# Performance work log

Measured on AMD Instinct MI355X. Metric: run time of the kernel, lower is better.

The kernel has to match this reference:

```python
import jax, jax.numpy as jnp
import numpy as np

B, S, N, D, NAMED, NTYPES = 8, 64, 100, 1024, 768, 5

def _ln(x, g, b, eps=1e-5):
    m = x.mean(-1, keepdims=True)
    v = ((x - m) ** 2).mean(-1, keepdims=True)
    return (x - m) * jax.lax.rsqrt(v + eps) * g + b

def _lin(x, W, b=None):
    y = x @ W.T
    return y if b is None else y + b

def setup_inputs():
    key = jax.random.key(0)
    ks = jax.random.split(key, 24)
    p = lambda i, shape, s=0.02: jax.random.normal(ks[i], shape, jnp.float32) * s
    inp = {}
    inp['scene_reps'] = jax.random.normal(ks[0], (B, S, D), jnp.float32)
    u = jax.random.uniform(ks[1], (B, N, S))
    keep = (jax.random.uniform(ks[2], (B, N, S)) < 0.25).astype(jnp.float32)
    inp['incidence_matrix'] = u * keep
    inp['edge_type_ids'] = jax.random.randint(ks[3], (B, S), 0, NTYPES)
    inp['entity_type_ids'] = jax.random.randint(ks[4], (B, N), 0, NTYPES)
    inp['entity_mask'] = jax.random.uniform(ks[5], (B, N)) < 0.9
    inp['entity_name_embs'] = jax.random.normal(ks[6], (B, N, NAMED), jnp.float32)
    inp['type_embed'] = p(7, (NTYPES, D), 1.0)
    inp['name_W'] = p(8, (D, NAMED))
    inp['name_ln_g'] = jnp.ones(D); inp['name_ln_b'] = jnp.zeros(D)
    inp['n2e_W'] = p(9, (D, D)); inp['n2e_b'] = jnp.zeros(D)
    inp['t2e_W'] = p(10, (D, D)); inp['t2e_b'] = jnp.zeros(D)
    inp['edge_ln_g'] = jnp.ones(D); inp['edge_ln_b'] = jnp.zeros(D)
    inp['gate_W1'] = p(11, (D // 4, D)); inp['gate_b1'] = jnp.zeros(D // 4)
    inp['gate_W2'] = p(12, (3, D // 4)); inp['gate_b2'] = jnp.zeros(3)
    inp['ms_W'] = p(13, (D, D)); inp['ms_b'] = jnp.zeros(D)
    inp['ma_W'] = p(14, (D, D)); inp['ma_b'] = jnp.zeros(D)
    inp['mi_W'] = p(15, (D, D)); inp['mi_b'] = jnp.zeros(D)
    inp['role_w'] = p(16, (D,))
    inp['gru_Wih'] = p(17, (3 * D, D)); inp['gru_Whh'] = p(18, (3 * D, D))
    inp['gru_bih'] = jnp.zeros(3 * D); inp['gru_bhh'] = jnp.zeros(3 * D)
    inp['upd_ln_g'] = jnp.ones(D); inp['upd_ln_b'] = jnp.zeros(D)
    inp['eo_W'] = p(19, (D, D)); inp['eo_b'] = jnp.zeros(D)
    inp['eo_ln_g'] = jnp.ones(D); inp['eo_ln_b'] = jnp.zeros(D)
    inp['res_ln_g'] = jnp.ones(D); inp['res_ln_b'] = jnp.zeros(D)
    return inp

def reference(scene_reps, incidence_matrix, edge_type_ids, entity_type_ids, entity_mask, entity_name_embs, type_embed, name_W, name_ln_g, name_ln_b, n2e_W, n2e_b, t2e_W, t2e_b, edge_ln_g, edge_ln_b, gate_W1, gate_b1, gate_W2, gate_b2, ms_W, ms_b, ma_W, ma_b, mi_W, mi_b, role_w, gru_Wih, gru_Whh, gru_bih, gru_bhh, upd_ln_g, upd_ln_b, eo_W, eo_b, eo_ln_g, eo_ln_b, res_ln_g, res_ln_b):
    # edge_type_ids is accepted by the torch module but unused in its forward.
    dt = scene_reps.dtype
    emaskf = entity_mask.astype(dt)  # [B,N]
    h0 = type_embed[entity_type_ids] + _ln(_lin(entity_name_embs, name_W), name_ln_g, name_ln_b)
    h0 = h0 * emaskf[..., None]
    eye = jnp.eye(N, dtype=dt)
    step_ids = jnp.arange(S)

    def step(carry, xs):
        h, ebuf = carry  # h [B,N,D], ebuf [B,S,D] (hyperedge history)
        s, x_s, inc_s = xs  # x_s [B,D], inc_s [B,N]
        roles = inc_s * emaskf
        wsum = jnp.maximum(roles.sum(1, keepdims=True), 1.0)
        mean_ent = jnp.einsum('bn,bnd->bd', roles, h) / wsum
        e_s = _ln(_lin(mean_ent, n2e_W, n2e_b) + _lin(x_s, t2e_W, t2e_b), edge_ln_g, edge_ln_b)
        in_mask = (roles > 0).astype(dt)[..., None]  # [B,N,1]
        msg_scene = _lin(e_s, ms_W, ms_b)[:, None, :]
        # arc stream: attention over past hyperedges with exponential recency decay
        valid = (step_ids < s).astype(dt)
        denom = jnp.maximum(s - 1, 1).astype(dt)
        decay = jnp.exp(-1.0 + step_ids.astype(dt) / denom) * valid  # linspace(-1,0,s)
        arc = incidence_matrix * roles[:, :, None] * decay[None, None, :]  # [B,N,S]
        arc = arc / jnp.maximum(arc.sum(-1, keepdims=True), 1e-8)
        msg_arc = _lin(jnp.einsum('bns,bsd->bnd', arc, jax.lax.stop_gradient(ebuf)), ma_W, ma_b)
        msg_arc = jnp.where(s > 0, msg_arc, jnp.zeros_like(msg_arc))
        # interaction stream: entity co-occurrence within the scene
        co = roles[:, :, None] * roles[:, None, :] * (1.0 - eye)
        co = co / jnp.maximum(co.sum(-1, keepdims=True), 1e-8)
        msg_int = _lin(jnp.einsum('bnm,bmd->bnd', co, h), mi_W, mi_b)
        gate = jax.nn.softmax(_lin(jax.nn.gelu(_lin(e_s, gate_W1, gate_b1), approximate=False), gate_W2, gate_b2), axis=-1)  # [B,3]
        msg = gate[:, 0, None, None] * msg_scene + gate[:, 1, None, None] * msg_arc + gate[:, 2, None, None] * msg_int
        msg = msg + (roles[..., None] * role_w) * in_mask
        # GRUCell (torch semantics) + LayerNorm, masked update
        gi = _lin(msg, gru_Wih, gru_bih)
        gh = _lin(h, gru_Whh, gru_bhh)
        i_r, i_z, i_n = jnp.split(gi, 3, axis=-1)
        h_r, h_z, h_n = jnp.split(gh, 3, axis=-1)
        r = jax.nn.sigmoid(i_r + h_r)
        z = jax.nn.sigmoid(i_z + h_z)
        n = jnp.tanh(i_n + r * h_n)
        h_new = jnp.clip(_ln((1 - z) * n + z * h, upd_ln_g, upd_ln_b), -50.0, 50.0)
        h = h * (1 - in_mask) + h_new * in_mask
        ebuf = ebuf.at[:, s].set(e_s)
        return (h, ebuf), e_s

    ebuf0 = jnp.zeros((B, S, D), dt)
    (h_fin, _), es = jax.lax.scan(step, (h0, ebuf0), (step_ids, scene_reps.transpose(1, 0, 2), incidence_matrix.transpose(2, 0, 1)))
    H = es.transpose(1, 0, 2)  # [B,S,D]
    H = _ln(H + scene_reps, res_ln_g, res_ln_b)
    H = _ln(jax.nn.gelu(_lin(H, eo_W, eo_b), approximate=False), eo_ln_g, eo_ln_b)
    return (H, h_fin)
```

## Files before the change

kernel.cpp:

```cpp
#include <hip/hip_runtime.h>
#include <math.h>

#define B_   8
#define S_   64
#define N_   100
#define D_   1024
#define ND_  768
#define BN_  800
#define G3_  3072
#define G6_  6144
#define RSC  0.00390625f

typedef _Float16 f16x8 __attribute__((ext_vector_type(8)));
typedef float f32x4 __attribute__((ext_vector_type(4)));

#define MFMA16(a,b,c) __builtin_amdgcn_mfma_f32_16x16x32_f16(a, b, c, 0, 0, 0)

static __device__ __forceinline__ float wave_sum(float v) {
    for (int off = 32; off > 0; off >>= 1) v += __shfl_down(v, off, 64);
    return v;
}

static __device__ __forceinline__ float block_sum(float v) {
    __shared__ float red_[8];
    float w = wave_sum(v);
    int lane = threadIdx.x & 63, wid = threadIdx.x >> 6;
    __syncthreads();
    if (lane == 0) red_[wid] = w;
    __syncthreads();
    float t = 0.f;
    for (int i = 0; i < 4; ++i) t += red_[i];
    return t;
}

static __device__ __forceinline__ float gelu_f(float x) {
    return 0.5f * x * (1.f + erff(x * 0.70710678118654752f));
}

static __device__ __forceinline__ unsigned short f2h(float x) {
    union { _Float16 h; unsigned short u; } c; c.h = (_Float16)x; return c.u;
}

__global__ __launch_bounds__(256) void k_f2h(
    const float* __restrict__ src, unsigned short* __restrict__ dst,
    int rows, int cols, int ldd)
{
    size_t n = (size_t)rows * cols;
    size_t i = ((size_t)blockIdx.x * 256 + threadIdx.x) * 4;
    if (i >= n) return;
    int r = (int)(i / cols);
    int c = (int)(i - (size_t)r * cols);
    float4 v = *(const float4*)(src + i);
    ushort4 o; o.x = f2h(v.x); o.y = f2h(v.y); o.z = f2h(v.z); o.w = f2h(v.w);
    *(ushort4*)(dst + (size_t)r * ldd + c) = o;
}

__global__ __launch_bounds__(256) void k_f2hT(
    const float* __restrict__ src, unsigned short* __restrict__ dst,
    int R, int C, int ldd, int rowoff)
{
    __shared__ _Float16 T[32][33];
    int tr = threadIdx.x >> 3, tc4 = (threadIdx.x & 7) * 4;
    int r0 = blockIdx.y * 32, c0 = blockIdx.x * 32;
    float4 v = *(const float4*)(src + (size_t)(r0 + tr) * C + c0 + tc4);
    T[tc4][tr] = (_Float16)v.x; T[tc4+1][tr] = (_Float16)v.y;
    T[tc4+2][tr] = (_Float16)v.z; T[tc4+3][tr] = (_Float16)v.w;
    __syncthreads();
    union { _Float16 h; unsigned short u; } cv;
    ushort4 o;
    cv.h = T[tr][tc4];   o.x = cv.u;
    cv.h = T[tr][tc4+1]; o.y = cv.u;
    cv.h = T[tr][tc4+2]; o.z = cv.u;
    cv.h = T[tr][tc4+3]; o.w = cv.u;
    *(ushort4*)(dst + (size_t)(rowoff + c0 + tr) * ldd + r0 + tc4) = o;
}

__global__ __launch_bounds__(256) void k_mfma16_nt(
    const unsigned short* __restrict__ A16, const unsigned short* __restrict__ W16,
    const float* __restrict__ bias, float* __restrict__ C,
    unsigned short* __restrict__ C16, float oscale,
    int M, int Nc, int K)
{
    int m0 = blockIdx.y * 64; if (m0 >= M) return;
    int n0 = blockIdx.x * 128;
    __shared__ _Float16 sA[64][72];
    __shared__ _Float16 sB[128][72];
    int tid = threadIdx.x;
    int w = tid >> 6, l = tid & 63;
    int l15 = l & 15, q = l >> 4;
    int wn = w * 32;
    int arow = tid >> 3, achk = (tid & 7) * 8;
    f32x4 acc[4][2] = {};
    for (int k0 = 0; k0 < K; k0 += 64) {
        for (int ri = 0; ri < 64; ri += 32) {
            int gm = m0 + arow + ri;
            uint4 v = make_uint4(0u, 0u, 0u, 0u);
            if (gm < M) v = *(const uint4*)(A16 + (size_t)gm * K + k0 + achk);
            *(uint4*)(&sA[arow + ri][achk]) = v;
        }
        for (int i = 0; i < 4; ++i) {
            int r = arow + 32 * i;
            *(uint4*)(&sB[r][achk]) = *(const uint4*)(W16 + (size_t)(n0 + r) * K + k0 + achk);
        }
        __syncthreads();
#pragma unroll
        for (int ks = 0; ks < 64; ks += 32) {
            f16x8 b0 = *(const f16x8*)(&sB[wn + l15][ks + q*8]);
            f16x8 b1 = *(const f16x8*)(&sB[wn + 16 + l15][ks + q*8]);
#pragma unroll
            for (int mi = 0; mi < 4; ++mi) {
                f16x8 a = *(const f16x8*)(&sA[mi*16 + l15][ks + q*8]);
                acc[mi][0] = MFMA16(a, b0, acc[mi][0]);
                acc[mi][1] = MFMA16(a, b1, acc[mi][1]);
            }
        }
        __syncthreads();
    }
    for (int mi = 0; mi < 4; ++mi)
        for (int nj = 0; nj < 2; ++nj)
            for (int r = 0; r < 4; ++r) {
                int gm = m0 + mi*16 + q*4 + r;
                int cl = wn + nj*16 + l15;
                if (gm < M) {
                    size_t off = (size_t)gm * Nc + n0 + cl;
                    float v = acc[mi][nj][r];
                    if (C16) C16[off] = f2h(v * oscale);
                    else C[off] = v + (bias ? bias[n0 + cl] : 0.f);
                }
            }
}

__global__ __launch_bounds__(256) void k_h0(
    const float* __restrict__ P, const int* __restrict__ etype,
    const int* __restrict__ emask, const float* __restrict__ temb,
    const float* __restrict__ g, const float* __restrict__ bt,
    float* __restrict__ h, unsigned short* __restrict__ h16)
{
    int bn = blockIdx.x, tid = threadIdx.x;
    int t = etype[bn], mk = emask[bn];
    float x[4]; float lsum = 0.f;
    for (int k = 0; k < 4; ++k) { x[k] = P[(size_t)bn*D_ + tid + 256*k]; lsum += x[k]; }
    float mean = block_sum(lsum) * (1.f / D_);
    float lv = 0.f;
    for (int k = 0; k < 4; ++k) { float d = x[k] - mean; lv += d * d; }
    float inv = rsqrtf(block_sum(lv) * (1.f / D_) + 1e-5f);
    for (int k = 0; k < 4; ++k) {
        int d = tid + 256*k;
        float y = (x[k] - mean) * inv * g[d] + bt[d];
        float hv = mk ? (temb[(size_t)t*D_ + d] + y) : 0.f;
        h[(size_t)bn*D_ + d] = hv;
        h16[(size_t)bn*D_ + d] = f2h(hv);
    }
}

__global__ __launch_bounds__(256) void k_step1(
    const float* __restrict__ inc, const int* __restrict__ emask,
    const float* __restrict__ h, const float* __restrict__ Esmi,
    float* __restrict__ ctxi, float* __restrict__ arcsum,
    int* __restrict__ cntp, int* __restrict__ lst, float* __restrict__ rro,
    const int* __restrict__ prevcnt, const int* __restrict__ prevlist,
    const unsigned short* __restrict__ h16, const unsigned short* __restrict__ n2e16,
    float* __restrict__ Hn, float* __restrict__ gatepre, int s)
{
    int tid = threadIdx.x, bid = blockIdx.x;
    if (bid == 0 && tid < 32) gatepre[tid] = 0.f;
    if (bid < BN_) {
        int m = bid;
        int b = m / N_, n = m - b * N_;
        float r = emask[m] ? inc[(size_t)m*S_ + s] : 0.f;
        if (r <= 0.f) return;
        __shared__ int sidx, nwa, nwi;
        __shared__ float wav[S_]; __shared__ int wai[S_];
        __shared__ float wiv[N_]; __shared__ int wii[N_];
        if (tid == 0) { sidx = atomicAdd(cntp, 1); nwa = 0; nwi = 0; }
        __syncthreads();
        int idx = sidx;
        if (tid == 0) { lst[idx] = m; rro[idx] = r; }
        float denomA = fmaxf((float)(s - 1), 1.f);
        float wa = 0.f;
        if (tid < s) {
            float iv = inc[(size_t)m*S_ + tid];
            if (iv > 0.f) {
                wa = iv * r * expf(-1.f + (float)tid / denomA);
                int p = atomicAdd(&nwa, 1);
                wav[p] = wa; wai[p] = tid;
            }
        }
        float dA = block_sum(wa);
        float wi = 0.f;
        if (tid < N_ && tid != n) {
            float rm = emask[b*N_ + tid] ? inc[((size_t)b*N_ + tid)*S_ + s] : 0.f;
            if (rm > 0.f) {
                wi = r * rm;
                int p = atomicAdd(&nwi, 1);
                wiv[p] = wi; wii[p] = tid;
            }
        }
        float dI = block_sum(wi);
        __syncthreads();
        int na = nwa, ni = nwi;
        float sclA = 1.f / fmaxf(dA, 1e-8f);
        float sclI = 1.f / fmaxf(dI, 1e-8f);
        float4 ii = make_float4(0.f,0.f,0.f,0.f);
        for (int j = 0; j < ni; ++j) {
            float wj = wiv[j];
            float4 v = *((const float4*)(h + ((size_t)b*N_ + wii[j])*D_) + tid);
            ii.x += wj*v.x; ii.y += wj*v.y; ii.z += wj*v.z; ii.w += wj*v.w;
        }
        ii.x *= sclI; ii.y *= sclI; ii.z *= sclI; ii.w *= sclI;
        *((float4*)(ctxi + (size_t)idx*D_) + tid) = ii;
        float a12[12];
#pragma unroll
        for (int k = 0; k < 12; ++k) a12[k] = 0.f;
        for (int j = 0; j < na; ++j) {
            float wj = wav[j];
            const float* ep = Esmi + ((size_t)b*S_ + wai[j])*G3_;
#pragma unroll
            for (int k = 0; k < 12; ++k) a12[k] += wj * ep[tid + 256*k];
        }
        float* ao = arcsum + (size_t)idx*G3_;
#pragma unroll
        for (int k = 0; k < 12; ++k) ao[tid + 256*k] = a12[k] * sclA;
    } else {
        int pM = *prevcnt;
        int t = bid - BN_;
        int n0 = (t & 15) * 64;
        int m0 = (t >> 4) * 32;
        if (m0 >= pM) return;
        __shared__ _Float16 sA[32][72];
        __shared__ _Float16 sB[64][72];
        __shared__ int slist[32];
        if (tid < 32) {
            int gm = m0 + tid;
            slist[tid] = (gm < pM) ? prevlist[gm] : 0;
        }
        __syncthreads();
        int w = tid >> 6, l = tid & 63;
        int l15 = l & 15, q = l >> 4;
        int wm = (w & 1) * 16, wn = (w >> 1) * 32;
        int arow = tid >> 3, achk = (tid & 7) * 8;
        int gmA = m0 + arow;
        f32x4 acc[2] = {};
        for (int k0 = 0; k0 < D_; k0 += 64) {
            {
                uint4 v = make_uint4(0u,0u,0u,0u);
                if (gmA < pM) v = *(const uint4*)(h16 + (size_t)slist[arow]*D_ + k0 + achk);
                *(uint4*)(&sA[arow][achk]) = v;
            }
            *(uint4*)(&sB[arow][achk])      = *(const uint4*)(n2e16 + (size_t)(n0 + arow)*D_ + k0 + achk);
            *(uint4*)(&sB[arow + 32][achk]) = *(const uint4*)(n2e16 + (size_t)(n0 + arow + 32)*D_ + k0 + achk);
            __syncthreads();
#pragma unroll
            for (int ks = 0; ks < 64; ks += 32) {
                f16x8 a  = *(const f16x8*)(&sA[wm + l15][ks + q*8]);
                f16x8 b0 = *(const f16x8*)(&sB[wn + l15][ks + q*8]);
                f16x8 b1 = *(const f16x8*)(&sB[wn + 16 + l15][ks + q*8]);
                acc[0] = MFMA16(a, b0, acc[0]);
                acc[1] = MFMA16(a, b1, acc[1]);
            }
            __syncthreads();
        }
        for (int j = 0; j < 2; ++j)
            for (int r = 0; r < 4; ++r) {
                int row = wm + q*4 + r;
                int gm = m0 + row;
                if (gm < pM)
                    Hn[(size_t)slist[row]*D_ + n0 + wn + j*16 + l15] = acc[j][r];
            }
    }
}

__global__ __launch_bounds__(256) void k_egate(
    const float* __restrict__ inc, const int* __restrict__ emask,
    const float* __restrict__ Hn, const float* __restrict__ n2eb,
    const float* __restrict__ pre_t2e,
    const float* __restrict__ elng, const float* __restrict__ elnb,
    const float* __restrict__ gW1, const float* __restrict__ gb1,
    const float* __restrict__ gW2,
    float* __restrict__ esbuf, float* __restrict__ gatepre,
    int* __restrict__ ctrl, int par, int s)
{
    int b = blockIdx.x, seg = blockIdx.y, tid = threadIdx.x;
    if (b == 0 && seg == 0 && tid == 0) ctrl[1 - par] = 0;
    __shared__ float sw[N_]; __shared__ int sidxn[N_]; __shared__ int snact;
    __shared__ float se[D_];
    if (tid == 0) snact = 0;
    __syncthreads();
    float r = 0.f;
    if (tid < N_) {
        r = emask[b*N_ + tid] ? inc[((size_t)b*N_ + tid)*S_ + s] : 0.f;
        if (r > 0.f) {
            int p = atomicAdd(&snact, 1);
            sw[p] = r; sidxn[p] = tid;
        }
    }
    float wsum = block_sum(r);
    int nact = snact;
    float invw = 1.f / fmaxf(wsum, 1.f);
    float4 e = make_float4(0.f,0.f,0.f,0.f);
    for (int j = 0; j < nact; ++j) {
        float wj = sw[j];
        float4 v = *((const float4*)(Hn + ((size_t)b*N_ + sidxn[j])*D_) + tid);
        e.x += wj*v.x; e.y += wj*v.y; e.z += wj*v.z; e.w += wj*v.w;
    }
    float4 nb = *((const float4*)n2eb + tid);
    float4 pt = *((const float4*)(pre_t2e + ((size_t)b*S_ + s)*D_) + tid);
    float x[4];
    x[0] = e.x*invw + nb.x + pt.x; x[1] = e.y*invw + nb.y + pt.y;
    x[2] = e.z*invw + nb.z + pt.z; x[3] = e.w*invw + nb.w + pt.w;
    float lsum = x[0] + x[1] + x[2] + x[3];
    float mean = block_sum(lsum) * (1.f / D_);
    float lv = 0.f;
    for (int k = 0; k < 4; ++k) { float d = x[k] - mean; lv += d * d; }
    float inv = rsqrtf(block_sum(lv) * (1.f / D_) + 1e-5f);
    float4 lg = *((const float4*)elng + tid);
    float4 lb = *((const float4*)elnb + tid);
    float y0 = (x[0]-mean)*inv*lg.x + lb.x;
    float y1 = (x[1]-mean)*inv*lg.y + lb.y;
    float y2 = (x[2]-mean)*inv*lg.z + lb.z;
    float y3 = (x[3]-mean)*inv*lg.w + lb.w;
    int d4 = tid * 4;
    se[d4] = y0; se[d4+1] = y1; se[d4+2] = y2; se[d4+3] = y3;
    if (seg == 0)
        *((float4*)(esbuf + ((size_t)b*S_ + s)*D_) + tid) = make_float4(y0,y1,y2,y3);
    __syncthreads();
    if (tid < 64) {
        int u = seg * 64 + tid;
        float acc = gb1[u];
        const float* w1 = gW1 + (size_t)u * D_;
        for (int j = 0; j < D_; j += 4) {
            float4 w = *(const float4*)(w1 + j);
            acc += w.x*se[j] + w.y*se[j+1] + w.z*se[j+2] + w.w*se[j+3];
        }
        float hg = gelu_f(acc);
        for (int c = 0; c < 3; ++c) {
            float p = wave_sum(gW2[c*256 + u] * hg);
            if (tid == 0) atomicAdd(gatepre + b*4 + c, p);
        }
    }
}

__global__ __launch_bounds__(256) void k_gemm_step(
    const float* __restrict__ ctxi, const float* __restrict__ esbuf,
    const unsigned short* __restrict__ h16,
    const int* __restrict__ lst, const int* __restrict__ cntp,
    const float* __restrict__ gatepre, const float* __restrict__ gb2,
    const unsigned short* __restrict__ Wmi16, const unsigned short* __restrict__ Whh16,
    const float* __restrict__ bhh, float* __restrict__ gig,
    float* __restrict__ Emi, float* __restrict__ Esmi, int s)
{
    int M = *cntp;
    int X = blockIdx.x, tid = threadIdx.x;
    int kind = (X < 48) ? 0 : (X < 96 ? 1 : 2);
    int m0 = blockIdx.y * 32;
    if (kind < 2) { if (m0 >= M) return; }
    else { if (blockIdx.y != 0) return; m0 = 0; }
    __shared__ _Float16 sA[32][72];
    __shared__ _Float16 sB[64][72];
    __shared__ float sg2[32];
    __shared__ int sbb[32];
    if (tid < 32) {
        int gm = m0 + tid;
        if (kind == 0) {
            float g2 = 0.f; int b = 0;
            if (gm < M) {
                b = lst[gm] / N_;
                float t0 = gatepre[b*4+0] + gb2[0];
                float t1 = gatepre[b*4+1] + gb2[1];
                float t2 = gatepre[b*4+2] + gb2[2];
                float mx = fmaxf(t0, fmaxf(t1, t2));
                float e0 = expf(t0-mx), e1 = expf(t1-mx), e2 = expf(t2-mx);
                g2 = e2 / (e0 + e1 + e2);
            }
            sg2[tid] = g2; sbb[tid] = b;
        } else if (kind == 1) {
            sbb[tid] = (gm < M) ? lst[gm] : 0;
        }
    }
    __syncthreads();
    int w = tid >> 6, l = tid & 63;
    int l15 = l & 15, q = l >> 4;
    int wm = (w & 1) * 16, wn = (w >> 1) * 32;
    int arow = tid >> 3, achk = (tid & 7) * 8;
    int gmA = m0 + arow;
    const unsigned short* Bp;
    int n0, ldb;
    if (kind == 0)      { n0 = X * 64;          Bp = Wmi16 + 2048; ldb = G3_; }
    else if (kind == 1) { n0 = (X - 48) * 64;   Bp = Whh16;        ldb = D_;  }
    else { int xo = X - 96; n0 = (xo % 48) * 64; Bp = Wmi16 + (xo / 48) * 1024; ldb = G3_; }
    f32x4 acc[2] = {};
    for (int k0 = 0; k0 < D_; k0 += 64) {
        {
            uint4 va = make_uint4(0u,0u,0u,0u);
            if (kind == 0) {
                if (gmA < M) {
                    float4 p0 = *(const float4*)(ctxi + (size_t)gmA*D_ + k0 + achk);
                    float4 p1 = *(const float4*)(ctxi + (size_t)gmA*D_ + k0 + achk + 4);
                    float sc = sg2[arow];
                    union { _Float16 hh[8]; uint4 u; } cv;
                    cv.hh[0] = (_Float16)(p0.x*sc); cv.hh[1] = (_Float16)(p0.y*sc);
                    cv.hh[2] = (_Float16)(p0.z*sc); cv.hh[3] = (_Float16)(p0.w*sc);
                    cv.hh[4] = (_Float16)(p1.x*sc); cv.hh[5] = (_Float16)(p1.y*sc);
                    cv.hh[6] = (_Float16)(p1.z*sc); cv.hh[7] = (_Float16)(p1.w*sc);
                    va = cv.u;
                }
            } else if (kind == 1) {
                if (gmA < M) va = *(const uint4*)(h16 + (size_t)sbb[arow]*D_ + k0 + achk);
            } else {
                if (arow < B_) {
                    const float* base = esbuf + ((size_t)arow*S_ + s)*D_ + k0 + achk;
                    float4 p0 = *(const float4*)(base);
                    float4 p1 = *(const float4*)(base + 4);
                    union { _Float16 hh[8]; uint4 u; } cv;
                    cv.hh[0] = (_Float16)p0.x; cv.hh[1] = (_Float16)p0.y;
                    cv.hh[2] = (_Float16)p0.z; cv.hh[3] = (_Float16)p0.w;
                    cv.hh[4] = (_Float16)p1.x; cv.hh[5] = (_Float16)p1.y;
                    cv.hh[6] = (_Float16)p1.z; cv.hh[7] = (_Float16)p1.w;
                    va = cv.u;
                }
            }
            *(uint4*)(&sA[arow][achk]) = va;
        }
        *(uint4*)(&sB[arow][achk])      = *(const uint4*)(Bp + (size_t)(n0 + arow)*ldb + k0 + achk);
        *(uint4*)(&sB[arow + 32][achk]) = *(const uint4*)(Bp + (size_t)(n0 + arow + 32)*ldb + k0 + achk);
        __syncthreads();
#pragma unroll
        for (int ks = 0; ks < 64; ks += 32) {
            f16x8 a  = *(const f16x8*)(&sA[wm + l15][ks + q*8]);
            f16x8 b0 = *(const f16x8*)(&sB[wn + l15][ks + q*8]);
            f16x8 b1 = *(const f16x8*)(&sB[wn + 16 + l15][ks + q*8]);
            acc[0] = MFMA16(a, b0, acc[0]);
            acc[1] = MFMA16(a, b1, acc[1]);
        }
        __syncthreads();
    }
    for (int j = 0; j < 2; ++j)
        for (int r = 0; r < 4; ++r) {
            int row = wm + q*4 + r;
            int gm = m0 + row;
            int cl = wn + j*16 + l15;
            if (kind == 0) {
                if (gm < M) gig[(size_t)gm * G6_ + n0 + cl] = acc[j][r];
            } else if (kind == 1) {
                if (gm < M) gig[(size_t)gm * G6_ + G3_ + n0 + cl] = acc[j][r] + bhh[n0 + cl];
            } else {
                if (row < B_) {
                    int xo = X - 96;
                    if (xo < 48) Emi[(size_t)row * G3_ + n0 + cl] = acc[j][r];
                    else Esmi[((size_t)row * S_ + s) * G3_ + n0 + cl] = acc[j][r];
                }
            }
        }
}

__global__ __launch_bounds__(256) void k_fin(
    const float* __restrict__ gig,
    const int* __restrict__ lst, const int* __restrict__ cntp,
    const float* __restrict__ ulng, const float* __restrict__ ulnb,
    const float* __restrict__ Emi, const float* __restrict__ arcsum,
    const float* __restrict__ gatepre, const float* __restrict__ gb2,
    const float* __restrict__ gBm, const float* __restrict__ bih,
    const float* __restrict__ rro,
    float* __restrict__ h, unsigned short* __restrict__ h16, int s)
{
    int row = blockIdx.x;
    if (row >= *cntp) return;
    int bn = lst[row];
    int b = bn / N_;
    int tid = threadIdx.x;
    float t0 = gatepre[b*4+0] + gb2[0];
    float t1 = gatepre[b*4+1] + gb2[1];
    float t2 = gatepre[b*4+2] + gb2[2];
    float mx = fmaxf(t0, fmaxf(t1, t2));
    float e0 = expf(t0-mx), e1 = expf(t1-mx), e2 = expf(t2-mx);
    float si = 1.f / (e0 + e1 + e2);
    float g0 = e0*si, g1 = (s > 0) ? e1*si : 0.f, g2 = e2*si;
    float rv = rro[row];
    const float* gi = gig + (size_t)row * G6_;
    const float* gh = gi + G3_;
    const float* em = Emi + (size_t)b * G3_;
    const float* as = arcsum + (size_t)row * G3_;
    float u[4]; float lsum = 0.f;
    for (int k = 0; k < 4; ++k) {
        int d = tid + 256*k;
        float ip[3];
#pragma unroll
        for (int c = 0; c < 3; ++c) {
            int dd = c*D_ + d;
            ip[c] = RSC * (gi[dd] + g0*em[dd] + g1*as[dd])
                  + g0*gBm[dd] + g1*gBm[G3_ + dd] + g2*gBm[2*G3_ + dd]
                  + rv*gBm[3*G3_ + dd] + bih[dd];
        }
        float hr = gh[d], hz = gh[D_ + d], hn = gh[2*D_ + d];
        float hv = h[(size_t)bn*D_ + d];
        float r = 1.f / (1.f + expf(-(ip[0] + hr)));
        float z = 1.f / (1.f + expf(-(ip[1] + hz)));
        float nn = tanhf(ip[2] + r * hn);
        u[k] = (1.f - z) * nn + z * hv;
        lsum += u[k];
    }
    float mean = block_sum(lsum) * (1.f / D_);
    float lv = 0.f;
    for (int k = 0; k < 4; ++k) { float d = u[k] - mean; lv += d * d; }
    float inv = rsqrtf(block_sum(lv) * (1.f / D_) + 1e-5f);
    for (int k = 0; k < 4; ++k) {
        int d = tid + 256*k;
        float y = (u[k] - mean) * inv * ulng[d] + ulnb[d];
        y = fminf(fmaxf(y, -50.f), 50.f);
        h[(size_t)bn*D_ + d] = y;
        h16[(size_t)bn*D_ + d] = f2h(y);
    }
}

__global__ __launch_bounds__(256) void k_resln(
    float* __restrict__ buf, const float* __restrict__ scene,
    const float* __restrict__ g, const float* __restrict__ bt,
    unsigned short* __restrict__ H16)
{
    size_t row = blockIdx.x;
    int tid = threadIdx.x;
    float x[4]; float lsum = 0.f;
    for (int k = 0; k < 4; ++k) {
        int d = tid + 256*k;
        x[k] = buf[row*D_ + d] + scene[row*D_ + d];
        lsum += x[k];
    }
    float mean = block_sum(lsum) * (1.f / D_);
    float lv = 0.f;
    for (int k = 0; k < 4; ++k) { float d = x[k] - mean; lv += d * d; }
    float inv = rsqrtf(block_sum(lv) * (1.f / D_) + 1e-5f);
    for (int k = 0; k < 4; ++k) {
        int d = tid + 256*k;
        float y = (x[k] - mean) * inv * g[d] + bt[d];
        buf[row*D_ + d] = y;
        H16[row*D_ + d] = f2h(y);
    }
}

__global__ __launch_bounds__(256) void k_final(
    const float* __restrict__ G, const float* __restrict__ g, const float* __restrict__ bt,
    float* __restrict__ outH, const float* __restrict__ h, float* __restrict__ outh)
{
    int tid = threadIdx.x;
    if (blockIdx.x < B_*S_) {
        size_t row = blockIdx.x;
        float x[4]; float lsum = 0.f;
        for (int k = 0; k < 4; ++k) {
            x[k] = gelu_f(G[row*D_ + tid + 256*k]);
            lsum += x[k];
        }
        float mean = block_sum(lsum) * (1.f / D_);
        float lv = 0.f;
        for (int k = 0; k < 4; ++k) { float d = x[k] - mean; lv += d * d; }
        float inv = rsqrtf(block_sum(lv) * (1.f / D_) + 1e-5f);
        for (int k = 0; k < 4; ++k) {
            int d = tid + 256*k;
            outH[row*D_ + d] = (x[k] - mean) * inv * g[d] + bt[d];
        }
    } else {
        size_t bn = blockIdx.x - B_*S_;
        for (int d = tid; d < D_; d += 256)
            outh[bn*D_ + d] = h[bn*D_ + d];
    }
}

extern "C" void kernel_launch(void* const* d_in, const int* in_sizes, int n_in,
                              void* d_out, int out_size, void* d_ws, size_t ws_size,
                              hipStream_t stream)
{
    const float* scene = (const float*)d_in[0];
    const float* inc   = (const float*)d_in[1];
    const int*   etype = (const int*)d_in[3];
    const int*   emask = (const int*)d_in[4];
    const float* nemb  = (const float*)d_in[5];
    const float* temb  = (const float*)d_in[6];
    const float* nameW = (const float*)d_in[7];
    const float* nlg   = (const float*)d_in[8];
    const float* nlb   = (const float*)d_in[9];
    const float* n2eW  = (const float*)d_in[10];
    const float* n2eb  = (const float*)d_in[11];
    const float* t2eW  = (const float*)d_in[12];
    const float* t2eb  = (const float*)d_in[13];
    const float* elng  = (const float*)d_in[14];
    const float* elnb  = (const float*)d_in[15];
    const float* gW1   = (const float*)d_in[16];
    const float* gb1   = (const float*)d_in[17];
    const float* gW2   = (const float*)d_in[18];
    const float* gb2   = (const float*)d_in[19];
    const float* msW   = (const float*)d_in[20];
    const float* msB   = (const float*)d_in[21];
    const float* maW   = (const float*)d_in[22];
    const float* maB   = (const float*)d_in[23];
    const float* miW   = (const float*)d_in[24];
    const float* miB   = (const float*)d_in[25];
    const float* rolew = (const float*)d_in[26];
    const float* Wih   = (const float*)d_in[27];
    const float* Whh   = (const float*)d_in[28];
    const float* bih   = (const float*)d_in[29];
    const float* bhh   = (const float*)d_in[30];
    const float* ulng  = (const float*)d_in[31];
    const float* ulnb  = (const float*)d_in[32];
    const float* eoW   = (const float*)d_in[33];
    const float* eoB   = (const float*)d_in[34];
    const float* eolng = (const float*)d_in[35];
    const float* eolnb = (const float*)d_in[36];
    const float* rlng  = (const float*)d_in[37];
    const float* rlnb  = (const float*)d_in[38];

    float* outH = (float*)d_out;
    float* outh = outH + (size_t)B_*S_*D_;

    float* W = (float*)d_ws;
    size_t o = 0;
    int*   ctrl     = (int*)(W + o); o += 64;
    float* gatepre  = W + o; o += 32;
    float* rowrole  = W + o; o += 2*BN_;
    int*   list     = (int*)(W + o); o += 2*BN_;
    float* ctxi     = W + o; o += (size_t)BN_*D_;
    float* hbuf     = W + o; o += (size_t)BN_*D_;
    float* Hn       = W + o; o += (size_t)BN_*D_;
    float* pre_t2e  = W + o; o += (size_t)B_*S_*D_;
    float* gBm      = W + o; o += 4*G3_;
    float* Emi      = W + o; o += (size_t)B_*G3_;
    float* Esmi     = W + o; o += (size_t)B_*S_*G3_;
    float* arcsum   = W + o; o += (size_t)BN_*G3_;
    float* gig      = W + o; o += (size_t)BN_*G6_;
    unsigned short* U = (unsigned short*)(W + o);
    size_t uo = 0;
    unsigned short* h16    = U + uo; uo += (size_t)BN_*D_;
    unsigned short* H16    = U + uo; uo += (size_t)B_*S_*D_;
    unsigned short* Wih16  = U + uo; uo += (size_t)G3_*D_;
    unsigned short* Whh16  = U + uo; uo += (size_t)G3_*D_;
    unsigned short* n2e16  = U + uo; uo += (size_t)D_*D_;
    unsigned short* eoW16  = U + uo; uo += (size_t)D_*D_;
    unsigned short* nW16   = U + uo; uo += (size_t)D_*ND_;
    unsigned short* nE16   = U + uo; uo += (size_t)BN_*ND_;
    unsigned short* t2e16  = U + uo; uo += (size_t)D_*D_;
    unsigned short* sc16   = U + uo; uo += (size_t)B_*S_*D_;
    unsigned short* WcatT16= U + uo; uo += (size_t)G3_*D_;
    unsigned short* Wmi16  = U + uo; uo += (size_t)G3_*G3_;
    unsigned short* bias4  = U + uo; uo += 4*D_;

    hipMemsetAsync(ctrl, 0, 16, stream);

    #define CVT(src, dst, r, c, ld) \
        k_f2h<<<(((size_t)(r)*(c)/4 + 255)/256), 256, 0, stream>>>(src, dst, r, c, ld)
    CVT(Wih,   Wih16, G3_, D_,  D_);
    CVT(Whh,   Whh16, G3_, D_,  D_);
    CVT(n2eW,  n2e16, D_,  D_,  D_);
    CVT(nameW, nW16,  D_,  ND_, ND_);
    CVT(nemb,  nE16,  BN_, ND_, ND_);
    CVT(eoW,   eoW16, D_,  D_,  D_);
    CVT(t2eW,  t2e16, D_,  D_,  D_);
    CVT(scene, sc16,  B_*S_, D_, D_);
    CVT(msB,   bias4 + 0,    1, D_, D_);
    CVT(maB,   bias4 + D_,   1, D_, D_);
    CVT(miB,   bias4 + 2*D_, 1, D_, D_);
    CVT(rolew, bias4 + 3*D_, 1, D_, D_);
    #undef CVT
    k_f2hT<<<dim3(32,32), 256, 0, stream>>>(msW, WcatT16, D_, D_, D_, 0);
    k_f2hT<<<dim3(32,32), 256, 0, stream>>>(maW, WcatT16, D_, D_, D_, D_);
    k_f2hT<<<dim3(32,32), 256, 0, stream>>>(miW, WcatT16, D_, D_, D_, 2*D_);

    k_mfma16_nt<<<dim3(G3_/128, G3_/64), 256, 0, stream>>>(
        Wih16, WcatT16, nullptr, nullptr, Wmi16, 256.f, G3_, G3_, D_);
    k_mfma16_nt<<<dim3(G3_/128, 1), 256, 0, stream>>>(
        bias4, Wih16, nullptr, gBm, nullptr, 1.f, 4, G3_, D_);
    k_mfma16_nt<<<dim3(D_/128, (B_*S_+63)/64), 256, 0, stream>>>(
        sc16, t2e16, t2eb, pre_t2e, nullptr, 1.f, B_*S_, D_, D_);
    k_mfma16_nt<<<dim3(D_/128, (BN_+63)/64), 256, 0, stream>>>(
        nE16, nW16, nullptr, gig, nullptr, 1.f, BN_, D_, ND_);
    k_h0<<<BN_, 256, 0, stream>>>(gig, etype, emask, temb, nlg, nlb, hbuf, h16);
    k_mfma16_nt<<<dim3(D_/128, (BN_+63)/64), 256, 0, stream>>>(
        h16, n2e16, nullptr, Hn, nullptr, 1.f, BN_, D_, D_);

    for (int s = 0; s < S_; ++s) {
        int par = s & 1;
        int*   cntp = ctrl + par;
        int*   pcnt = ctrl + (1 - par);
        int*   lst  = list + par * BN_;
        int*   plst = list + (1 - par) * BN_;
        float* rro  = rowrole + par * BN_;
        k_step1<<<BN_ + 400, 256, 0, stream>>>(inc, emask, hbuf, Esmi,
            ctxi, arcsum, cntp, lst, rro, pcnt, plst, h16, n2e16, Hn, gatepre, s);
        k_egate<<<dim3(B_, 4), 256, 0, stream>>>(inc, emask, Hn, n2eb, pre_t2e,
            elng, elnb, gW1, gb1, gW2, outH, gatepre, ctrl, par, s);
        k_gemm_step<<<dim3(192, 25), 256, 0, stream>>>(ctxi, outH, h16,
            lst, cntp, gatepre, gb2, Wmi16, Whh16, bhh, gig, Emi, Esmi, s);
        k_fin<<<BN_, 256, 0, stream>>>(gig, lst, cntp, ulng, ulnb,
            Emi, arcsum, gatepre, gb2, gBm, bih, rro, hbuf, h16, s);
    }

    k_resln<<<B_*S_, 256, 0, stream>>>(outH, scene, rlng, rlnb, H16);
    k_mfma16_nt<<<dim3(D_/128, (B_*S_+63)/64), 256, 0, stream>>>(
        H16, eoW16, eoB, gig, nullptr, 1.f, B_*S_, D_, D_);
    k_final<<<B_*S_ + BN_, 256, 0, stream>>>(gig, eolng, eolnb, outH, hbuf, outh);
}
```

Baseline: 5.018 ms.

## Precompute per-entity h projections and replace interaction context with batch sum minus self

The per-entity projection of h now covers n2e, the interaction slice of the merged msg-to-GRU weight, and Whh in one concatenated 7168-wide output (Hcat). It is refreshed only for the rows updated in the previous step, inside the front kernel. The interaction message term becomes a per-batch weighted sum of projected rows minus the entity's own contribution, with scaling done in k_fin. This removes the per-step ctxi gather and the separate gemm_step kernel, cutting four launches per step to three. In exchange the incremental GEMM is wider (112 column tiles), and precision shifts because the interaction term is projected before weighting rather than after.

```diff
diff --git a/kernel.cpp b/kernel.cpp
--- a/kernel.cpp
+++ b/kernel.cpp
@@ -9,6 +9,7 @@
 #define BN_  800
 #define G3_  3072
 #define G6_  6144
+#define HC7  7168
 #define RSC  0.00390625f
 
 typedef _Float16 f16x8 __attribute__((ext_vector_type(8)));
@@ -153,29 +154,70 @@
     }
 }
 
-__global__ __launch_bounds__(256) void k_step1(
+__global__ __launch_bounds__(256) void k_hcat0(
+    const unsigned short* __restrict__ h16, const unsigned short* __restrict__ n2e16,
+    const unsigned short* __restrict__ Wmi16, const unsigned short* __restrict__ Whh16,
+    float* __restrict__ Hcat)
+{
+    int m0 = blockIdx.y * 32;
+    int n0 = blockIdx.x * 64;
+    const unsigned short* Bp; int ldb; int nl;
+    if (n0 < 1024)      { Bp = n2e16;        ldb = D_;  nl = n0; }
+    else if (n0 < 4096) { Bp = Wmi16 + 2048; ldb = G3_; nl = n0 - 1024; }
+    else                { Bp = Whh16;        ldb = D_;  nl = n0 - 4096; }
+    __shared__ _Float16 sA[32][72];
+    __shared__ _Float16 sB[64][72];
+    int tid = threadIdx.x;
+    int w = tid >> 6, l = tid & 63;
+    int l15 = l & 15, q = l >> 4;
+    int wm = (w & 1) * 16, wn = (w >> 1) * 32;
+    int arow = tid >> 3, achk = (tid & 7) * 8;
+    int gmA = m0 + arow;
+    f32x4 acc[2] = {};
+    for (int k0 = 0; k0 < D_; k0 += 64) {
+        *(uint4*)(&sA[arow][achk]) = *(const uint4*)(h16 + (size_t)gmA*D_ + k0 + achk);
+        *(uint4*)(&sB[arow][achk])      = *(const uint4*)(Bp + (size_t)(nl + arow)*ldb + k0 + achk);
+        *(uint4*)(&sB[arow + 32][achk]) = *(const uint4*)(Bp + (size_t)(nl + arow + 32)*ldb + k0 + achk);
+        __syncthreads();
+#pragma unroll
+        for (int ks = 0; ks < 64; ks += 32) {
+            f16x8 a  = *(const f16x8*)(&sA[wm + l15][ks + q*8]);
+            f16x8 b0 = *(const f16x8*)(&sB[wn + l15][ks + q*8]);
+            f16x8 b1 = *(const f16x8*)(&sB[wn + 16 + l15][ks + q*8]);
+            acc[0] = MFMA16(a, b0, acc[0]);
+            acc[1] = MFMA16(a, b1, acc[1]);
+        }
+        __syncthreads();
+    }
+    for (int j = 0; j < 2; ++j)
+        for (int r = 0; r < 4; ++r) {
+            int row = wm + q*4 + r;
+            Hcat[(size_t)(m0 + row)*HC7 + n0 + wn + j*16 + l15] = acc[j][r];
+        }
+}
+
+__global__ __launch_bounds__(256) void k_front(
     const float* __restrict__ inc, const int* __restrict__ emask,
-    const float* __restrict__ h, const float* __restrict__ Esmi,
-    float* __restrict__ ctxi, float* __restrict__ arcsum,
+    const float* __restrict__ Esmi, float* __restrict__ arcsum,
     int* __restrict__ cntp, int* __restrict__ lst, float* __restrict__ rro,
+    float* __restrict__ scl,
     const int* __restrict__ prevcnt, const int* __restrict__ prevlist,
     const unsigned short* __restrict__ h16, const unsigned short* __restrict__ n2e16,
-    float* __restrict__ Hn, float* __restrict__ gatepre, int s)
+    const unsigned short* __restrict__ Wmi16, const unsigned short* __restrict__ Whh16,
+    float* __restrict__ Hcat, float* __restrict__ gatepre, int s)
 {
     int tid = threadIdx.x, bid = blockIdx.x;
     if (bid == 0 && tid < 32) gatepre[tid] = 0.f;
     if (bid < BN_) {
         int m = bid;
-        int b = m / N_, n = m - b * N_;
+        int b = m / N_;
         float r = emask[m] ? inc[(size_t)m*S_ + s] : 0.f;
         if (r <= 0.f) return;
-        __shared__ int sidx, nwa, nwi;
+        __shared__ int sidx, nwa;
         __shared__ float wav[S_]; __shared__ int wai[S_];
-        __shared__ float wiv[N_]; __shared__ int wii[N_];
-        if (tid == 0) { sidx = atomicAdd(cntp, 1); nwa = 0; nwi = 0; }
+        if (tid == 0) { sidx = atomicAdd(cntp, 1); nwa = 0; }
         __syncthreads();
         int idx = sidx;
-        if (tid == 0) { lst[idx] = m; rro[idx] = r; }
         float denomA = fmaxf((float)(s - 1), 1.f);
         float wa = 0.f;
         if (tid < s) {
@@ -187,28 +229,16 @@
             }
         }
         float dA = block_sum(wa);
-        float wi = 0.f;
-        if (tid < N_ && tid != n) {
-            float rm = emask[b*N_ + tid] ? inc[((size_t)b*N_ + tid)*S_ + s] : 0.f;
-            if (rm > 0.f) {
-                wi = r * rm;
-                int p = atomicAdd(&nwi, 1);
-                wiv[p] = wi; wii[p] = tid;
-            }
-        }
-        float dI = block_sum(wi);
-        __syncthreads();
-        int na = nwa, ni = nwi;
+        float rm = 0.f;
+        if (tid < N_) rm = emask[b*N_ + tid] ? inc[((size_t)b*N_ + tid)*S_ + s] : 0.f;
+        float wsum = block_sum(rm);
+        __syncthreads();
+        int na = nwa;
         float sclA = 1.f / fmaxf(dA, 1e-8f);
-        float sclI = 1.f / fmaxf(dI, 1e-8f);
-        float4 ii = make_float4(0.f,0.f,0.f,0.f);
-        for (int j = 0; j < ni; ++j) {
-            float wj = wiv[j];
-            float4 v = *((const float4*)(h + ((size_t)b*N_ + wii[j])*D_) + tid);
-            ii.x += wj*v.x; ii.y += wj*v.y; ii.z += wj*v.z; ii.w += wj*v.w;
-        }
-        ii.x *= sclI; ii.y *= sclI; ii.z *= sclI; ii.w *= sclI;
-        *((float4*)(ctxi + (size_t)idx*D_) + tid) = ii;
+        if (tid == 0) {
+            lst[idx] = m; rro[idx] = r;
+            scl[idx] = r / fmaxf(r * (wsum - r), 1e-8f);
+        }
         float a12[12];
 #pragma unroll
         for (int k = 0; k < 12; ++k) a12[k] = 0.f;
@@ -224,9 +254,14 @@
     } else {
         int pM = *prevcnt;
         int t = bid - BN_;
-        int n0 = (t & 15) * 64;
-        int m0 = (t >> 4) * 32;
+        int nt = t % 112, mt = t / 112;
+        int m0 = mt * 32;
         if (m0 >= pM) return;
+        int n0 = nt * 64;
+        const unsigned short* Bp; int ldb; int nl;
+        if (n0 < 1024)      { Bp = n2e16;        ldb = D_;  nl = n0; }
+        else if (n0 < 4096) { Bp = Wmi16 + 2048; ldb = G3_; nl = n0 - 1024; }
+        else                { Bp = Whh16;        ldb = D_;  nl = n0 - 4096; }
         __shared__ _Float16 sA[32][72];
         __shared__ _Float16 sB[64][72];
         __shared__ int slist[32];
@@ -247,8 +282,8 @@
                 if (gmA < pM) v = *(const uint4*)(h16 + (size_t)slist[arow]*D_ + k0 + achk);
                 *(uint4*)(&sA[arow][achk]) = v;
             }
-            *(uint4*)(&sB[arow][achk])      = *(const uint4*)(n2e16 + (size_t)(n0 + arow)*D_ + k0 + achk);
-            *(uint4*)(&sB[arow + 32][achk]) = *(const uint4*)(n2e16 + (size_t)(n0 + arow + 32)*D_ + k0 + achk);
+            *(uint4*)(&sB[arow][achk])      = *(const uint4*)(Bp + (size_t)(nl + arow)*ldb + k0 + achk);
+            *(uint4*)(&sB[arow + 32][achk]) = *(const uint4*)(Bp + (size_t)(nl + arow + 32)*ldb + k0 + achk);
             __syncthreads();
 #pragma unroll
             for (int ks = 0; ks < 64; ks += 32) {
@@ -265,42 +300,38 @@
                 int row = wm + q*4 + r;
                 int gm = m0 + row;
                 if (gm < pM)
-                    Hn[(size_t)slist[row]*D_ + n0 + wn + j*16 + l15] = acc[j][r];
-            }
-    }
-}
-
-__global__ __launch_bounds__(256) void k_egate(
+                    Hcat[(size_t)slist[row]*HC7 + n0 + wn + j*16 + l15] = acc[j][r];
+            }
+    }
+}
+
+static __device__ void compute_es(
+    int b, int s,
     const float* __restrict__ inc, const int* __restrict__ emask,
-    const float* __restrict__ Hn, const float* __restrict__ n2eb,
+    const float* __restrict__ Hcat, const float* __restrict__ n2eb,
     const float* __restrict__ pre_t2e,
     const float* __restrict__ elng, const float* __restrict__ elnb,
-    const float* __restrict__ gW1, const float* __restrict__ gb1,
-    const float* __restrict__ gW2,
-    float* __restrict__ esbuf, float* __restrict__ gatepre,
-    int* __restrict__ ctrl, int par, int s)
-{
-    int b = blockIdx.x, seg = blockIdx.y, tid = threadIdx.x;
-    if (b == 0 && seg == 0 && tid == 0) ctrl[1 - par] = 0;
-    __shared__ float sw[N_]; __shared__ int sidxn[N_]; __shared__ int snact;
-    __shared__ float se[D_];
-    if (tid == 0) snact = 0;
+    float* se)
+{
+    __shared__ float sw_[N_]; __shared__ int sidx_[N_]; __shared__ int snact_;
+    int tid = threadIdx.x;
+    if (tid == 0) snact_ = 0;
     __syncthreads();
     float r = 0.f;
     if (tid < N_) {
         r = emask[b*N_ + tid] ? inc[((size_t)b*N_ + tid)*S_ + s] : 0.f;
         if (r > 0.f) {
-            int p = atomicAdd(&snact, 1);
-            sw[p] = r; sidxn[p] = tid;
+            int p = atomicAdd(&snact_, 1);
+            sw_[p] = r; sidx_[p] = tid;
         }
     }
     float wsum = block_sum(r);
-    int nact = snact;
+    int nact = snact_;
     float invw = 1.f / fmaxf(wsum, 1.f);
     float4 e = make_float4(0.f,0.f,0.f,0.f);
     for (int j = 0; j < nact; ++j) {
-        float wj = sw[j];
-        float4 v = *((const float4*)(Hn + ((size_t)b*N_ + sidxn[j])*D_) + tid);
+        float wj = sw_[j];
+        float4 v = *((const float4*)(Hcat + (size_t)(b*N_ + sidx_[j])*HC7) + tid);
         e.x += wj*v.x; e.y += wj*v.y; e.z += wj*v.z; e.w += wj*v.w;
     }
     float4 nb = *((const float4*)n2eb + tid);
@@ -315,152 +346,105 @@
     float inv = rsqrtf(block_sum(lv) * (1.f / D_) + 1e-5f);
     float4 lg = *((const float4*)elng + tid);
     float4 lb = *((const float4*)elnb + tid);
-    float y0 = (x[0]-mean)*inv*lg.x + lb.x;
-    float y1 = (x[1]-mean)*inv*lg.y + lb.y;
-    float y2 = (x[2]-mean)*inv*lg.z + lb.z;
-    float y3 = (x[3]-mean)*inv*lg.w + lb.w;
     int d4 = tid * 4;
-    se[d4] = y0; se[d4+1] = y1; se[d4+2] = y2; se[d4+3] = y3;
-    if (seg == 0)
-        *((float4*)(esbuf + ((size_t)b*S_ + s)*D_) + tid) = make_float4(y0,y1,y2,y3);
+    se[d4]   = (x[0]-mean)*inv*lg.x + lb.x;
+    se[d4+1] = (x[1]-mean)*inv*lg.y + lb.y;
+    se[d4+2] = (x[2]-mean)*inv*lg.z + lb.z;
+    se[d4+3] = (x[3]-mean)*inv*lg.w + lb.w;
     __syncthreads();
-    if (tid < 64) {
-        int u = seg * 64 + tid;
-        float acc = gb1[u];
-        const float* w1 = gW1 + (size_t)u * D_;
-        for (int j = 0; j < D_; j += 4) {
-            float4 w = *(const float4*)(w1 + j);
-            acc += w.x*se[j] + w.y*se[j+1] + w.z*se[j+2] + w.w*se[j+3];
-        }
-        float hg = gelu_f(acc);
-        for (int c = 0; c < 3; ++c) {
-            float p = wave_sum(gW2[c*256 + u] * hg);
-            if (tid == 0) atomicAdd(gatepre + b*4 + c, p);
-        }
-    }
-}
-
-__global__ __launch_bounds__(256) void k_gemm_step(
-    const float* __restrict__ ctxi, const float* __restrict__ esbuf,
-    const unsigned short* __restrict__ h16,
+}
+
+__global__ __launch_bounds__(256) void k_mid(
+    const float* __restrict__ inc, const int* __restrict__ emask,
+    const float* __restrict__ Hcat, const float* __restrict__ n2eb,
+    const float* __restrict__ pre_t2e,
+    const float* __restrict__ elng, const float* __restrict__ elnb,
+    const float* __restrict__ gW1, const float* __restrict__ gb1,
+    const float* __restrict__ gW2, const unsigned short* __restrict__ Wmi16,
+    float* __restrict__ esbuf, float* __restrict__ gatepre,
+    float* __restrict__ Tmi, float* __restrict__ Emi, float* __restrict__ Esmi,
+    int* __restrict__ ctrl, int par, int s)
+{
+    int bid = blockIdx.x, tid = threadIdx.x;
+    __shared__ float se[D_];
+    if (bid < 32) {
+        int b = bid >> 2, seg = bid & 3;
+        if (bid == 0 && tid == 0) ctrl[1 - par] = 0;
+        compute_es(b, s, inc, emask, Hcat, n2eb, pre_t2e, elng, elnb, se);
+        if (seg == 0) {
+            for (int k = 0; k < 4; ++k) {
+                int d = tid + 256*k;
+                esbuf[((size_t)b*S_ + s)*D_ + d] = se[d];
+            }
+        }
+        if (tid < 64) {
+            int u = seg * 64 + tid;
+            float acc = gb1[u];
+            const float* w1 = gW1 + (size_t)u * D_;
+            for (int j = 0; j < D_; j += 4) {
+                float4 w = *(const float4*)(w1 + j);
+                acc += w.x*se[j] + w.y*se[j+1] + w.z*se[j+2] + w.w*se[j+3];
+            }
+            float hg = gelu_f(acc);
+            for (int c = 0; c < 3; ++c) {
+                float p = wave_sum(gW2[c*256 + u] * hg);
+                if (tid == 0) atomicAdd(gatepre + b*4 + c, p);
+            }
+        }
+    } else if (bid < 128) {
+        int t = bid - 32;
+        int b = t / 12, ch = t - b*12;
+        __shared__ float sw_[N_]; __shared__ int sidx_[N_]; __shared__ int snact_;
+        if (tid == 0) snact_ = 0;
+        __syncthreads();
+        if (tid < N_) {
+            float r = emask[b*N_ + tid] ? inc[((size_t)b*N_ + tid)*S_ + s] : 0.f;
+            if (r > 0.f) {
+                int p = atomicAdd(&snact_, 1);
+                sw_[p] = r; sidx_[p] = tid;
+            }
+        }
+        __syncthreads();
+        int nact = snact_;
+        int col = ch * 256 + tid;
+        float acc = 0.f;
+        for (int j = 0; j < nact; ++j)
+            acc += sw_[j] * Hcat[(size_t)(b*N_ + sidx_[j])*HC7 + 1024 + col];
+        Tmi[(size_t)b*G3_ + col] = acc;
+    } else {
+        int t = bid - 128;
+        int b = t / 96, u = t - b*96;
+        int soff = (u >= 48) ? 1024 : 0;
+        int n0 = (u % 48) * 64;
+        compute_es(b, s, inc, emask, Hcat, n2eb, pre_t2e, elng, elnb, se);
+        int coll = tid >> 2, kq = (tid & 3) * 256;
+        int col = n0 + coll;
+        const unsigned short* pr = Wmi16 + (size_t)col * G3_ + soff + kq;
+        float acc = 0.f;
+        for (int kk = 0; kk < 256; kk += 8) {
+            uint4 pv = *(const uint4*)(pr + kk);
+            union { uint4 uu; _Float16 h[8]; } cv; cv.uu = pv;
+#pragma unroll
+            for (int j = 0; j < 8; ++j) acc += (float)cv.h[j] * se[kq + kk + j];
+        }
+        acc += __shfl_xor(acc, 1, 64);
+        acc += __shfl_xor(acc, 2, 64);
+        if ((tid & 3) == 0) {
+            if (soff == 0) Emi[(size_t)b*G3_ + col] = acc;
+            else Esmi[((size_t)b*S_ + s)*G3_ + col] = acc;
+        }
+    }
+}
+
+__global__ __launch_bounds__(256) void k_fin(
     const int* __restrict__ lst, const int* __restrict__ cntp,
+    const float* __restrict__ rro, const float* __restrict__ scl,
     const float* __restrict__ gatepre, const float* __restrict__ gb2,
-    const unsigned short* __restrict__ Wmi16, const unsigned short* __restrict__ Whh16,
-    const float* __restrict__ bhh, float* __restrict__ gig,
-    float* __restrict__ Emi, float* __restrict__ Esmi, int s)
-{
-    int M = *cntp;
-    int X = blockIdx.x, tid = threadIdx.x;
-    int kind = (X < 48) ? 0 : (X < 96 ? 1 : 2);
-    int m0 = blockIdx.y * 32;
-    if (kind < 2) { if (m0 >= M) return; }
-    else { if (blockIdx.y != 0) return; m0 = 0; }
-    __shared__ _Float16 sA[32][72];
-    __shared__ _Float16 sB[64][72];
-    __shared__ float sg2[32];
-    __shared__ int sbb[32];
-    if (tid < 32) {
-        int gm = m0 + tid;
-        if (kind == 0) {
-            float g2 = 0.f; int b = 0;
-            if (gm < M) {
-                b = lst[gm] / N_;
-                float t0 = gatepre[b*4+0] + gb2[0];
-                float t1 = gatepre[b*4+1] + gb2[1];
-                float t2 = gatepre[b*4+2] + gb2[2];
-                float mx = fmaxf(t0, fmaxf(t1, t2));
-                float e0 = expf(t0-mx), e1 = expf(t1-mx), e2 = expf(t2-mx);
-                g2 = e2 / (e0 + e1 + e2);
-            }
-            sg2[tid] = g2; sbb[tid] = b;
-        } else if (kind == 1) {
-            sbb[tid] = (gm < M) ? lst[gm] : 0;
-        }
-    }
-    __syncthreads();
-    int w = tid >> 6, l = tid & 63;
-    int l15 = l & 15, q = l >> 4;
-    int wm = (w & 1) * 16, wn = (w >> 1) * 32;
-    int arow = tid >> 3, achk = (tid & 7) * 8;
-    int gmA = m0 + arow;
-    const unsigned short* Bp;
-    int n0, ldb;
-    if (kind == 0)      { n0 = X * 64;          Bp = Wmi16 + 2048; ldb = G3_; }
-    else if (kind == 1) { n0 = (X - 48) * 64;   Bp = Whh16;        ldb = D_;  }
-    else { int xo = X - 96; n0 = (xo % 48) * 64; Bp = Wmi16 + (xo / 48) * 1024; ldb = G3_; }
-    f32x4 acc[2] = {};
-    for (int k0 = 0; k0 < D_; k0 += 64) {
-        {
-            uint4 va = make_uint4(0u,0u,0u,0u);
-            if (kind == 0) {
-                if (gmA < M) {
-                    float4 p0 = *(const float4*)(ctxi + (size_t)gmA*D_ + k0 + achk);
-                    float4 p1 = *(const float4*)(ctxi + (size_t)gmA*D_ + k0 + achk + 4);
-                    float sc = sg2[arow];
-                    union { _Float16 hh[8]; uint4 u; } cv;
-                    cv.hh[0] = (_Float16)(p0.x*sc); cv.hh[1] = (_Float16)(p0.y*sc);
-                    cv.hh[2] = (_Float16)(p0.z*sc); cv.hh[3] = (_Float16)(p0.w*sc);
-                    cv.hh[4] = (_Float16)(p1.x*sc); cv.hh[5] = (_Float16)(p1.y*sc);
-                    cv.hh[6] = (_Float16)(p1.z*sc); cv.hh[7] = (_Float16)(p1.w*sc);
-                    va = cv.u;
-                }
-            } else if (kind == 1) {
-                if (gmA < M) va = *(const uint4*)(h16 + (size_t)sbb[arow]*D_ + k0 + achk);
-            } else {
-                if (arow < B_) {
-                    const float* base = esbuf + ((size_t)arow*S_ + s)*D_ + k0 + achk;
-                    float4 p0 = *(const float4*)(base);
-                    float4 p1 = *(const float4*)(base + 4);
-                    union { _Float16 hh[8]; uint4 u; } cv;
-                    cv.hh[0] = (_Float16)p0.x; cv.hh[1] = (_Float16)p0.y;
-                    cv.hh[2] = (_Float16)p0.z; cv.hh[3] = (_Float16)p0.w;
-                    cv.hh[4] = (_Float16)p1.x; cv.hh[5] = (_Float16)p1.y;
-                    cv.hh[6] = (_Float16)p1.z; cv.hh[7] = (_Float16)p1.w;
-                    va = cv.u;
-                }
-            }
-            *(uint4*)(&sA[arow][achk]) = va;
-        }
-        *(uint4*)(&sB[arow][achk])      = *(const uint4*)(Bp + (size_t)(n0 + arow)*ldb + k0 + achk);
-        *(uint4*)(&sB[arow + 32][achk]) = *(const uint4*)(Bp + (size_t)(n0 + arow + 32)*ldb + k0 + achk);
-        __syncthreads();
-#pragma unroll
-        for (int ks = 0; ks < 64; ks += 32) {
-            f16x8 a  = *(const f16x8*)(&sA[wm + l15][ks + q*8]);
-            f16x8 b0 = *(const f16x8*)(&sB[wn + l15][ks + q*8]);
-            f16x8 b1 = *(const f16x8*)(&sB[wn + 16 + l15][ks + q*8]);
-            acc[0] = MFMA16(a, b0, acc[0]);
-            acc[1] = MFMA16(a, b1, acc[1]);
-        }
-        __syncthreads();
-    }
-    for (int j = 0; j < 2; ++j)
-        for (int r = 0; r < 4; ++r) {
-            int row = wm + q*4 + r;
-            int gm = m0 + row;
-            int cl = wn + j*16 + l15;
-            if (kind == 0) {
-                if (gm < M) gig[(size_t)gm * G6_ + n0 + cl] = acc[j][r];
-            } else if (kind == 1) {
-                if (gm < M) gig[(size_t)gm * G6_ + G3_ + n0 + cl] = acc[j][r] + bhh[n0 + cl];
-            } else {
-                if (row < B_) {
-                    int xo = X - 96;
-                    if (xo < 48) Emi[(size_t)row * G3_ + n0 + cl] = acc[j][r];
-                    else Esmi[((size_t)row * S_ + s) * G3_ + n0 + cl] = acc[j][r];
-                }
-            }
-        }
-}
-
-__global__ __launch_bounds__(256) void k_fin(
-    const float* __restrict__ gig,
-    const int* __restrict__ lst, const int* __restrict__ cntp,
+    const float* __restrict__ Hcat, const float* __restrict__ Emi,
+    const float* __restrict__ arcsum, const float* __restrict__ Tmi,
+    const float* __restrict__ gBm, const float* __restrict__ bih,
+    const float* __restrict__ bhh,
     const float* __restrict__ ulng, const float* __restrict__ ulnb,
-    const float* __restrict__ Emi, const float* __restrict__ arcsum,
-    const float* __restrict__ gatepre, const float* __restrict__ gb2,
-    const float* __restrict__ gBm, const float* __restrict__ bih,
-    const float* __restrict__ rro,
     float* __restrict__ h, unsigned short* __restrict__ h16, int s)
 {
     int row = blockIdx.x;
@@ -476,10 +460,11 @@
     float si = 1.f / (e0 + e1 + e2);
     float g0 = e0*si, g1 = (s > 0) ? e1*si : 0.f, g2 = e2*si;
     float rv = rro[row];
-    const float* gi = gig + (size_t)row * G6_;
-    const float* gh = gi + G3_;
+    float sI = scl[row];
+    const float* Hrow = Hcat + (size_t)bn * HC7;
     const float* em = Emi + (size_t)b * G3_;
     const float* as = arcsum + (size_t)row * G3_;
+    const float* tm = Tmi + (size_t)b * G3_;
     float u[4]; float lsum = 0.f;
     for (int k = 0; k < 4; ++k) {
         int d = tid + 256*k;
@@ -487,11 +472,14 @@
 #pragma unroll
         for (int c = 0; c < 3; ++c) {
             int dd = c*D_ + d;
-            ip[c] = RSC * (gi[dd] + g0*em[dd] + g1*as[dd])
+            float gint = tm[dd] - rv * Hrow[1024 + dd];
+            ip[c] = RSC * (g0*em[dd] + g1*as[dd] + g2*sI*gint)
                   + g0*gBm[dd] + g1*gBm[G3_ + dd] + g2*gBm[2*G3_ + dd]
                   + rv*gBm[3*G3_ + dd] + bih[dd];
         }
-        float hr = gh[d], hz = gh[D_ + d], hn = gh[2*D_ + d];
+        float hr = Hrow[4096 + d]        + bhh[d];
+        float hz = Hrow[4096 + D_ + d]   + bhh[D_ + d];
+        float hn = Hrow[4096 + 2*D_ + d] + bhh[2*D_ + d];
         float hv = h[(size_t)bn*D_ + d];
         float r = 1.f / (1.f + expf(-(ip[0] + hr)));
         float z = 1.f / (1.f + expf(-(ip[1] + hz)));
@@ -615,16 +603,17 @@
     int*   ctrl     = (int*)(W + o); o += 64;
     float* gatepre  = W + o; o += 32;
     float* rowrole  = W + o; o += 2*BN_;
+    float* sclbuf   = W + o; o += BN_;
     int*   list     = (int*)(W + o); o += 2*BN_;
-    float* ctxi     = W + o; o += (size_t)BN_*D_;
     float* hbuf     = W + o; o += (size_t)BN_*D_;
-    float* Hn       = W + o; o += (size_t)BN_*D_;
+    float* Hcat     = W + o; o += (size_t)BN_*HC7;
     float* pre_t2e  = W + o; o += (size_t)B_*S_*D_;
     float* gBm      = W + o; o += 4*G3_;
     float* Emi      = W + o; o += (size_t)B_*G3_;
     float* Esmi     = W + o; o += (size_t)B_*S_*G3_;
     float* arcsum   = W + o; o += (size_t)BN_*G3_;
-    float* gig      = W + o; o += (size_t)BN_*G6_;
+    float* Tmi      = W + o; o += (size_t)B_*G3_;
+    float* tmp      = W + o; o += (size_t)BN_*D_;
     unsigned short* U = (unsigned short*)(W + o);
     size_t uo = 0;
     unsigned short* h16    = U + uo; uo += (size_t)BN_*D_;
@@ -669,10 +658,9 @@
     k_mfma16_nt<<<dim3(D_/128, (B_*S_+63)/64), 256, 0, stream>>>(
         sc16, t2e16, t2eb, pre_t2e, nullptr, 1.f, B_*S_, D_, D_);
     k_mfma16_nt<<<dim3(D_/128, (BN_+63)/64), 256, 0, stream>>>(
-        nE16, nW16, nullptr, gig, nullptr, 1.f, BN_, D_, ND_);
-    k_h0<<<BN_, 256, 0, stream>>>(gig, etype, emask, temb, nlg, nlb, hbuf, h16);
-    k_mfma16_nt<<<dim3(D_/128, (BN_+63)/64), 256, 0, stream>>>(
-        h16, n2e16, nullptr, Hn, nullptr, 1.f, BN_, D_, D_);
+        nE16, nW16, nullptr, tmp, nullptr, 1.f, BN_, D_, ND_);
+    k_h0<<<BN_, 256, 0, stream>>>(tmp, etype, emask, temb, nlg, nlb, hbuf, h16);
+    k_hcat0<<<dim3(112, 25), 256, 0, stream>>>(h16, n2e16, Wmi16, Whh16, Hcat);
 
     for (int s = 0; s < S_; ++s) {
         int par = s & 1;
@@ -681,18 +669,18 @@
         int*   lst  = list + par * BN_;
         int*   plst = list + (1 - par) * BN_;
         float* rro  = rowrole + par * BN_;
-        k_step1<<<BN_ + 400, 256, 0, stream>>>(inc, emask, hbuf, Esmi,
-            ctxi, arcsum, cntp, lst, rro, pcnt, plst, h16, n2e16, Hn, gatepre, s);
-        k_egate<<<dim3(B_, 4), 256, 0, stream>>>(inc, emask, Hn, n2eb, pre_t2e,
-            elng, elnb, gW1, gb1, gW2, outH, gatepre, ctrl, par, s);
-        k_gemm_step<<<dim3(192, 25), 256, 0, stream>>>(ctxi, outH, h16,
-            lst, cntp, gatepre, gb2, Wmi16, Whh16, bhh, gig, Emi, Esmi, s);
-        k_fin<<<BN_, 256, 0, stream>>>(gig, lst, cntp, ulng, ulnb,
-            Emi, arcsum, gatepre, gb2, gBm, bih, rro, hbuf, h16, s);
+        k_front<<<BN_ + 112*25, 256, 0, stream>>>(inc, emask, Esmi, arcsum,
+            cntp, lst, rro, sclbuf, pcnt, plst, h16, n2e16, Wmi16, Whh16,
+            Hcat, gatepre, s);
+        k_mid<<<896, 256, 0, stream>>>(inc, emask, Hcat, n2eb, pre_t2e,
+            elng, elnb, gW1, gb1, gW2, Wmi16, outH, gatepre, Tmi, Emi, Esmi,
+            ctrl, par, s);
+        k_fin<<<BN_, 256, 0, stream>>>(lst, cntp, rro, sclbuf, gatepre, gb2,
+            Hcat, Emi, arcsum, Tmi, gBm, bih, bhh, ulng, ulnb, hbuf, h16, s);
     }
 
     k_resln<<<B_*S_, 256, 0, stream>>>(outH, scene, rlng, rlnb, H16);
     k_mfma16_nt<<<dim3(D_/128, (B_*S_+63)/64), 256, 0, stream>>>(
-        H16, eoW16, eoB, gig, nullptr, 1.f, B_*S_, D_, D_);
-    k_final<<<B_*S_ + BN_, 256, 0, stream>>>(gig, eolng, eolnb, outH, hbuf, outh);
-}
+        H16, eoW16, eoB, tmp, nullptr, 1.f, B_*S_, D_, D_);
+    k_final<<<B_*S_ + BN_, 256, 0, stream>>>(tmp, eolng, eolnb, outH, hbuf, outh);
+}
```

After: 4.202 ms. -16.3%, faster.
